# Kernel optimization log

Measured on AMD Instinct MI355X. Metric: run time of the kernel, lower is better.

Reference implementation:

```python
import jax, jax.numpy as jnp
import numpy as np

B, NUM, LQ, LP, H = 8, 4, 128, 512, 512


def setup_inputs() -> dict:
    key = jax.random.key(0)
    k1, k2, k3 = jax.random.split(key, 3)
    return {
        "encode_input1": jax.random.normal(k1, (B, NUM, LQ, H), jnp.float32),
        "encode_input2": jax.random.normal(k2, (B, NUM, LP, H), jnp.float32),
        "input1_mask": jnp.ones((B, NUM, LQ), jnp.int32),
        "input2_mask": jnp.ones((B, NUM, LP), jnp.int32),
        "w": jax.random.normal(k3, (3 * H,), jnp.float32) * (1.0 / np.sqrt(3 * H)),
    }


def reference(encode_input1, encode_input2, input1_mask, input2_mask, w):
    Bb, num_q, Lq, Hh = encode_input1.shape
    _, num_p, Lp, _ = encode_input2.shape
    # num_q == num_p path of the original module
    E_q = encode_input1.reshape(-1, Lq, Hh)            # [BM, Lq, H]
    E_p = encode_input2.reshape(-1, Lp, Hh)            # [BM, Lp, H]
    m_q = input1_mask.reshape(-1, Lq)
    m_p = input2_mask.reshape(-1, Lp)
    # Linear([E_q, E_p, E_q*E_p]) -> scalar decomposes into three terms;
    # avoids materializing the O(Lp*Lq*3H) broadcast-concat tensor.
    w_q, w_p, w_m = w[:Hh], w[Hh:2 * Hh], w[2 * Hh:]
    U = ((E_p @ w_p)[:, :, None]
         + (E_q @ w_q)[:, None, :]
         + jnp.einsum('bph,h,bqh->bpq', E_p, w_m, E_q))   # [BM, Lp, Lq]
    mask = (m_p[:, :, None] * m_q[:, None, :]).astype(bool)
    Um = jnp.where(mask, U, jnp.finfo(U.dtype).min)
    A_p = jnp.where(mask, jax.nn.softmax(Um, axis=2), 0.0)   # row softmax over Lq
    B_p = jnp.where(mask, jax.nn.softmax(Um, axis=1), 0.0)   # col softmax over Lp
    A1 = A_p @ E_q                                   # [BM, Lp, H]
    B1 = jnp.einsum('bpq,bph->bqh', B_p, E_p)        # [BM, Lq, H]
    A2 = A_p @ B1                                    # [BM, Lp, H]
    B2 = jnp.einsum('bpq,bph->bqh', B_p, A1)         # [BM, Lq, H]
    shp_p = (Bb, num_p, Lp, Hh)
    shp_q = (Bb, num_p, Lq, Hh)
    E_p4 = E_p.reshape(shp_p); E_q4 = E_q.reshape(shp_q)
    A1 = A1.reshape(shp_p); A2 = A2.reshape(shp_p)
    B1 = B1.reshape(shp_q); B2 = B2.reshape(shp_q)
    G_q_p = jnp.concatenate([E_p4, A1, A2, E_p4 * A1, E_p4 * A2], axis=-1)
    G_p_q = jnp.concatenate([E_q4, B1, B2, E_q4 * B1, E_q4 * B2], axis=-1)
    G_p_q = G_p_q * input1_mask[..., None].astype(G_p_q.dtype)
    G_q_p = G_q_p * input2_mask[..., None].astype(G_q_p.dtype)
    return (G_p_q, G_q_p)
```

## Files before the change

### kernel.cpp

```cpp
#include <hip/hip_runtime.h>
#include <hip/hip_bf16.h>

#define BBATCH 32
#define LQ 128
#define LP 512
#define HDIM 512
#define GDIM 2560
#define NEG_MAX (-3.402823466e38f)

typedef __attribute__((ext_vector_type(8))) short short8;
typedef __attribute__((ext_vector_type(4))) float f32x4;
typedef __attribute__((ext_vector_type(4))) unsigned short ushort4v;

__device__ inline unsigned short f2bf(float f) {
  union { float f; unsigned int u; } v; v.f = f;
  unsigned int r = v.u + 0x7FFFu + ((v.u >> 16) & 1u);
  return (unsigned short)(r >> 16);
}
__device__ inline float bf2f(unsigned short s) {
  union { unsigned int u; float f; } v; v.u = (unsigned int)s << 16;
  return v.f;
}

__device__ inline void stage128x64(const unsigned short* __restrict__ src, int ld,
                                   int row0, int k0, unsigned short* lds, int t) {
#pragma unroll
  for (int i = 0; i < 4; i++) {
    int o = (t + i * 256) * 16;
    int row = o >> 7, col = (o & 127) >> 1;
    int swz = o ^ ((row & 7) << 4);
    *(short8*)((char*)lds + swz) = *(const short8*)(src + (long)(row0 + row) * ld + k0 + col);
  }
}
__device__ inline void stage64x64_f32(const float* __restrict__ src, int ld,
                                      int row0, int k0, unsigned short* lds, int t) {
#pragma unroll
  for (int i = 0; i < 2; i++) {
    int o = (t + i * 256) * 16;
    int row = o >> 7, col = (o & 127) >> 1;
    int swz = o ^ ((row & 7) << 4);
    const float* p = src + (long)(row0 + row) * ld + k0 + col;
    float4 a = *(const float4*)p;
    float4 b2 = *(const float4*)(p + 4);
    short8 v = {(short)f2bf(a.x), (short)f2bf(a.y), (short)f2bf(a.z), (short)f2bf(a.w),
                (short)f2bf(b2.x), (short)f2bf(b2.y), (short)f2bf(b2.z), (short)f2bf(b2.w)};
    *(short8*)((char*)lds + swz) = v;
  }
}
__device__ inline short8 fragld(const unsigned short* lds, int row, int ks, int fq) {
  return *(const short8*)((const char*)lds + (((row << 7) + ks * 64 + fq * 16) ^ ((row & 7) << 4)));
}

__global__ __launch_bounds__(256) void prep_kernel(
    const float* __restrict__ Ep, const float* __restrict__ Eq,
    const float* __restrict__ w,
    unsigned short* __restrict__ EpT, unsigned short* __restrict__ EqT,
    unsigned short* __restrict__ Eqw,
    float* __restrict__ epv, float* __restrict__ eqv) {
  const int b = blockIdx.y;
  const int bx = blockIdx.x;
  const bool isP = bx < 8;
  const int R = isP ? LP : LQ;
  const int p0 = (isP ? bx : bx - 8) * 64;
  const float* src = isP ? Ep + (long)b * LP * HDIM : Eq + (long)b * LQ * HDIM;
  const float* wb_base = isP ? w + HDIM : w;
  unsigned short* dT = isP ? EpT + (long)b * HDIM * LP : EqT + (long)b * HDIM * LQ;
  unsigned short* dW = isP ? nullptr : Eqw + (long)b * LQ * HDIM;
  float* bias = (isP ? epv + b * LP : eqv + b * LQ) + p0;
  __shared__ float T[64][65];
  const int t = threadIdx.x, c4 = (t & 15) * 4, r = t >> 4;
  float dot[4] = {0.f, 0.f, 0.f, 0.f};
  for (int h0 = 0; h0 < HDIM; h0 += 64) {
    float4 wb = *(const float4*)(wb_base + h0 + c4);
    float4 wm4 = {0, 0, 0, 0};
    if (!isP) wm4 = *(const float4*)(w + 2 * HDIM + h0 + c4);
    __syncthreads();
#pragma unroll
    for (int i = 0; i < 4; i++) {
      int row = r + 16 * i;
      float4 v = *(const float4*)(src + (long)(p0 + row) * HDIM + h0 + c4);
      T[row][c4] = v.x; T[row][c4 + 1] = v.y; T[row][c4 + 2] = v.z; T[row][c4 + 3] = v.w;
      if (!isP) {
        ushort4v ow = {f2bf(v.x * wm4.x), f2bf(v.y * wm4.y), f2bf(v.z * wm4.z), f2bf(v.w * wm4.w)};
        *(ushort4v*)(dW + (long)(p0 + row) * HDIM + h0 + c4) = ow;
      }
      dot[i] += v.x * wb.x + v.y * wb.y + v.z * wb.z + v.w * wb.w;
    }
    __syncthreads();
#pragma unroll
    for (int i = 0; i < 4; i++) {
      int hh = r + 16 * i;
      ushort4v o = {f2bf(T[c4][hh]), f2bf(T[c4 + 1][hh]), f2bf(T[c4 + 2][hh]), f2bf(T[c4 + 3][hh])};
      *(ushort4v*)(dT + (long)(h0 + hh) * R + p0 + c4) = o;
    }
  }
#pragma unroll
  for (int i = 0; i < 4; i++) {
#pragma unroll
    for (int s = 1; s < 16; s <<= 1) dot[i] += __shfl_xor(dot[i], s);
  }
  if ((t & 15) == 0) {
#pragma unroll
    for (int i = 0; i < 4; i++) bias[r + 16 * i] = dot[i];
  }
}

__global__ __launch_bounds__(256) void u_gemm(
    const float* __restrict__ EpF, const unsigned short* __restrict__ Bb,
    const float* __restrict__ epv, const float* __restrict__ eqv,
    const int* __restrict__ maskM, const int* __restrict__ maskN,
    float* __restrict__ UmT, unsigned short* __restrict__ Apb) {
  const int hw = blockIdx.x;
  const int xcd = hw & 7, s_ = hw >> 3;
  const int b = xcd * 4 + (s_ >> 3);
  const int m0 = (s_ & 7) * 64;
  const float* A = EpF + (long)b * LP * HDIM;
  const unsigned short* B = Bb + (long)b * LQ * HDIM;
  __shared__ unsigned short As[4096];
  __shared__ unsigned short Bs[8192];
  __shared__ float smax[2][64], ssum[2][64];
  const int t = threadIdx.x, lane = t & 63, wid = t >> 6;
  const int wm = wid >> 1, wn = wid & 1;
  const int wr = wm * 32, wc = wn * 64;
  const int fr = lane & 15, fq = lane >> 4;
  f32x4 acc[2][4] = {};
  for (int k0 = 0; k0 < HDIM; k0 += 64) {
    stage64x64_f32(A, HDIM, m0, k0, As, t);
    stage128x64(B, HDIM, 0, k0, Bs, t);
    __syncthreads();
#pragma unroll
    for (int ks = 0; ks < 2; ks++) {
      short8 af[2], bfv[4];
#pragma unroll
      for (int i = 0; i < 2; i++) af[i] = fragld(As, wr + i * 16 + fr, ks, fq);
#pragma unroll
      for (int j = 0; j < 4; j++) bfv[j] = fragld(Bs, wc + j * 16 + fr, ks, fq);
#pragma unroll
      for (int i = 0; i < 2; i++)
#pragma unroll
        for (int j = 0; j < 4; j++)
          acc[i][j] = __builtin_amdgcn_mfma_f32_16x16x32_bf16(af[i], bfv[j], acc[i][j], 0, 0, 0);
    }
    __syncthreads();
  }
  const float* ep_b = epv + (long)b * LP;
  const float* eq_b = eqv + (long)b * LQ;
  const int* mM = maskM + (long)b * LP;
  const int* mN = maskN + (long)b * LQ;
  float* UmTB = UmT + (long)b * LQ * LP;
  unsigned short* ApB = Apb + (long)b * LP * LQ;
  float eqc[4]; int mnc[4];
#pragma unroll
  for (int j = 0; j < 4; j++) {
    int col = wc + j * 16 + fr;
    eqc[j] = eq_b[col]; mnc[j] = mN[col];
  }
  float epr[2][4]; int mmr[2][4];
#pragma unroll
  for (int i = 0; i < 2; i++)
#pragma unroll
    for (int r = 0; r < 4; r++) {
      int row = m0 + wr + i * 16 + fq * 4 + r;
      epr[i][r] = ep_b[row]; mmr[i][r] = mM[row];
    }
#pragma unroll
  for (int i = 0; i < 2; i++)
#pragma unroll
    for (int j = 0; j < 4; j++) {
      float4 tv;
#pragma unroll
      for (int r = 0; r < 4; r++) {
        float a = acc[i][j][r];
        bool ok = mmr[i][r] && mnc[j];
        ((float*)&tv)[r] = ok ? a + epr[i][r] : NEG_MAX;
        acc[i][j][r] = ok ? a + eqc[j] : NEG_MAX;
      }
      int col = wc + j * 16 + fr;
      *(float4*)(UmTB + (long)col * LP + m0 + wr + i * 16 + fq * 4) = tv;
    }
  float mx[2][4];
#pragma unroll
  for (int i = 0; i < 2; i++)
#pragma unroll
    for (int r = 0; r < 4; r++) {
      float m = fmaxf(fmaxf(acc[i][0][r], acc[i][1][r]), fmaxf(acc[i][2][r], acc[i][3][r]));
#pragma unroll
      for (int s = 1; s < 16; s <<= 1) m = fmaxf(m, __shfl_xor(m, s));
      mx[i][r] = m;
      if (fr == 0) smax[wn][wr + i * 16 + fq * 4 + r] = m;
    }
  __syncthreads();
#pragma unroll
  for (int i = 0; i < 2; i++)
#pragma unroll
    for (int r = 0; r < 4; r++) {
      int rl = wr + i * 16 + fq * 4 + r;
      mx[i][r] = fmaxf(smax[0][rl], smax[1][rl]);
    }
#pragma unroll
  for (int i = 0; i < 2; i++)
#pragma unroll
    for (int r = 0; r < 4; r++) {
      float s = 0.f;
#pragma unroll
      for (int j = 0; j < 4; j++) {
        float e = __expf(acc[i][j][r] - mx[i][r]);
        acc[i][j][r] = e; s += e;
      }
#pragma unroll
      for (int sh = 1; sh < 16; sh <<= 1) s += __shfl_xor(s, sh);
      if (fr == 0) ssum[wn][wr + i * 16 + fq * 4 + r] = s;
    }
  __syncthreads();
#pragma unroll
  for (int i = 0; i < 2; i++)
#pragma unroll
    for (int r = 0; r < 4; r++) {
      int rl = wr + i * 16 + fq * 4 + r;
      float S = ssum[0][rl] + ssum[1][rl];
      float inv = S > 0.f ? 1.f / S : 0.f;
      int row = m0 + rl;
#pragma unroll
      for (int j = 0; j < 4; j++) {
        int col = wc + j * 16 + fr;
        bool ok = mmr[i][r] && mnc[j];
        ApB[(long)row * LQ + col] = ok ? f2bf(acc[i][j][r] * inv) : 0;
      }
    }
}

__global__ __launch_bounds__(256) void colsoftmaxT_kernel(
    const float* __restrict__ UmT, unsigned short* __restrict__ BpT,
    const int* __restrict__ mp, const int* __restrict__ mq) {
  int wid = blockIdx.x * 4 + (threadIdx.x >> 6);
  int lane = threadIdx.x & 63;
  int b = wid >> 7;
  const float* row = UmT + (long)wid * LP;
  float v[8];
  float m = NEG_MAX;
#pragma unroll
  for (int i = 0; i < 8; i++) { v[i] = row[lane + 64 * i]; m = fmaxf(m, v[i]); }
#pragma unroll
  for (int off = 32; off; off >>= 1) m = fmaxf(m, __shfl_xor(m, off));
  float e[8];
  float s = 0.f;
#pragma unroll
  for (int i = 0; i < 8; i++) { e[i] = __expf(v[i] - m); s += e[i]; }
#pragma unroll
  for (int off = 32; off; off >>= 1) s += __shfl_xor(s, off);
  float inv = s > 0.f ? 1.f / s : 0.f;
  int mqv = mq[wid];
#pragma unroll
  for (int i = 0; i < 8; i++) {
    int p = lane + 64 * i;
    bool ok = mqv && mp[b * LP + p];
    BpT[(long)wid * LP + p] = ok ? f2bf(e[i] * inv) : 0;
  }
}

template <int PHASE>
__global__ __launch_bounds__(256) void gemm_phase(
    const unsigned short* __restrict__ Apb, const unsigned short* __restrict__ BpT,
    const unsigned short* __restrict__ BA, const unsigned short* __restrict__ BB,
    const float* __restrict__ EpF, const float* __restrict__ EqF,
    const int* __restrict__ mp, const int* __restrict__ mq,
    float* __restrict__ out_gqp, float* __restrict__ out_gpq,
    unsigned short* __restrict__ A1T, unsigned short* __restrict__ B1T) {
  const int hw = blockIdx.x;
  const int xcd = hw & 7, s_ = hw >> 3;
  const int b = xcd * 4 + (s_ / 20);
  const int bx = s_ % 20;
  __shared__ __align__(16) char smem[32768];
  unsigned short* As = (unsigned short*)smem;
  unsigned short* Bs = (unsigned short*)(smem + 16384);
  float (*Cs)[132] = (float(*)[132])smem;
  const int t = threadIdx.x, lane = t & 63, wid = t >> 6;
  const int wr = (wid >> 1) * 64, wc = (wid & 1) * 64;
  const int fr = lane & 15, fq = lane >> 4;
  const unsigned short* A; const unsigned short* Bop;
  int K, M, m0, n0;
  float* outBase; const float* Eb; const int* mb;
  unsigned short* Tout;
  if (bx < 4) {
    A = BpT + (long)b * LQ * LP; K = LP; M = LQ; m0 = 0; n0 = bx * 128;
    Bop = BB + (long)b * HDIM * LP;
    outBase = out_gpq + (long)b * LQ * GDIM;
    Eb = EqF + (long)b * LQ * HDIM; mb = mq + (long)b * LQ;
    Tout = (PHASE == 1) ? B1T + (long)b * HDIM * LQ : nullptr;
  } else {
    int idx = bx - 4; m0 = (idx >> 2) * 128; n0 = (idx & 3) * 128;
    A = Apb + (long)b * LP * LQ; K = LQ; M = LP;
    Bop = BA + (long)b * HDIM * LQ;
    outBase = out_gqp + (long)b * LP * GDIM;
    Eb = EpF + (long)b * LP * HDIM; mb = mp + (long)b * LP;
    Tout = (PHASE == 1) ? A1T + (long)b * HDIM * LP : nullptr;
  }
  f32x4 acc[4][4] = {};
  for (int k0 = 0; k0 < K; k0 += 64) {
    stage128x64(A, K, m0, k0, As, t);
    stage128x64(Bop, K, n0, k0, Bs, t);
    __syncthreads();
#pragma unroll
    for (int ks = 0; ks < 2; ks++) {
      short8 af[4], bfv[4];
#pragma unroll
      for (int i = 0; i < 4; i++) {
        af[i] = fragld(As, wr + i * 16 + fr, ks, fq);
        bfv[i] = fragld(Bs, wc + i * 16 + fr, ks, fq);
      }
#pragma unroll
      for (int i = 0; i < 4; i++)
#pragma unroll
        for (int j = 0; j < 4; j++)
          acc[i][j] = __builtin_amdgcn_mfma_f32_16x16x32_bf16(af[i], bfv[j], acc[i][j], 0, 0, 0);
    }
    __syncthreads();
  }
  if (PHASE == 1) {
#pragma unroll
    for (int i = 0; i < 4; i++)
#pragma unroll
      for (int j = 0; j < 4; j++) {
        int col = n0 + wc + j * 16 + fr;
        int row0 = m0 + wr + i * 16 + fq * 4;
        ushort4v o = {f2bf(acc[i][j][0]), f2bf(acc[i][j][1]),
                      f2bf(acc[i][j][2]), f2bf(acc[i][j][3])};
        *(ushort4v*)(Tout + (long)col * M + row0) = o;
      }
  }
  const int band = wid >> 1;
#pragma unroll
  for (int i = 0; i < 4; i++) {
    __syncthreads();
#pragma unroll
    for (int j = 0; j < 4; j++) {
#pragma unroll
      for (int r = 0; r < 4; r++)
        Cs[band * 16 + fq * 4 + r][wc + j * 16 + fr] = acc[i][j][r];
    }
    __syncthreads();
#pragma unroll
    for (int k = 0; k < 4; k++) {
      int slot = t + k * 256;
      int row_l = slot >> 5;
      int c4 = (slot & 31) * 4;
      int bnd = row_l >> 4;
      int r_g = m0 + bnd * 64 + i * 16 + (row_l & 15);
      float mm = (float)mb[r_g];
      f32x4 v = *(f32x4*)&Cs[row_l][c4];
      f32x4 e = *(const f32x4*)(Eb + (long)r_g * HDIM + n0 + c4);
      float* orow = outBase + (long)r_g * GDIM + n0 + c4;
      f32x4 vm = v * mm;
      f32x4 evm = e * vm;
      if (PHASE == 1) {
        __builtin_nontemporal_store(e * mm, (f32x4*)(orow));
        __builtin_nontemporal_store(vm, (f32x4*)(orow + HDIM));
        __builtin_nontemporal_store(evm, (f32x4*)(orow + 3 * HDIM));
      } else {
        __builtin_nontemporal_store(vm, (f32x4*)(orow + 2 * HDIM));
        __builtin_nontemporal_store(evm, (f32x4*)(orow + 4 * HDIM));
      }
    }
  }
}

extern "C" void kernel_launch(void* const* d_in, const int* in_sizes, int n_in,
                              void* d_out, int out_size, void* d_ws, size_t ws_size,
                              hipStream_t stream) {
  const float* Eq = (const float*)d_in[0];
  const float* Ep = (const float*)d_in[1];
  const int* mq = (const int*)d_in[2];
  const int* mp = (const int*)d_in[3];
  const float* w = (const float*)d_in[4];
  float* out = (float*)d_out;
  float* out_gpq = out;
  float* out_gqp = out + (long)BBATCH * LQ * GDIM;

  unsigned short* EpT = (unsigned short*)d_ws;
  unsigned short* EqT = EpT + 32L * 512 * 512;
  unsigned short* Eqw = EqT + 32L * 512 * 128;
  unsigned short* Apb = Eqw + 32L * 128 * 512;
  unsigned short* BpT = Apb + 32L * 512 * 128;
  unsigned short* B1T = BpT + 32L * 128 * 512;
  unsigned short* A1T = B1T + 32L * 512 * 128;
  float* UmT = (float*)(A1T + 32L * 512 * 512);
  float* epb = UmT + 32L * 128 * 512;
  float* eqb2 = epb + 32L * 512;

  prep_kernel<<<dim3(10, BBATCH), 256, 0, stream>>>(
      Ep, Eq, w, EpT, EqT, Eqw, epb, eqb2);

  u_gemm<<<dim3(256), 256, 0, stream>>>(
      Ep, Eqw, epb, eqb2, mp, mq, UmT, Apb);

  colsoftmaxT_kernel<<<BBATCH * LQ / 4, 256, 0, stream>>>(UmT, BpT, mp, mq);

  gemm_phase<1><<<dim3(640), 256, 0, stream>>>(
      Apb, BpT, EqT, EpT, Ep, Eq, mp, mq, out_gqp, out_gpq, A1T, B1T);

  gemm_phase<2><<<dim3(640), 256, 0, stream>>>(
      Apb, BpT, B1T, A1T, Ep, Eq, mp, mq, out_gqp, out_gpq, nullptr, nullptr);
}
```

Before: 107.2 us.

## Reassociate B2 as (Bp^T·Ap)·Eq to drop the A1 intermediate

Computes B2 as (B_p^T A_p) E_q instead of B_p^T (A_p E_q). The small 128x128 product is accumulated alongside B1 in the same K loop, staged in LDS as bf16, and multiplied by Eq^T inside the same block. This removes the A1T bf16 intermediate, which was written and then read back from global memory, and u_gemm now also writes a transposed copy of A_p. The G_p_q blocks now emit all five output slices in one kernel, and A2 moves to a separate smaller kernel. In exchange, the Bp^T·Ap product is recomputed redundantly by each of the four column blocks per batch, those blocks become heavier, which risks load imbalance, and LDS use rises to 64 KB.

```diff
diff --git a/kernel.cpp b/kernel.cpp
--- a/kernel.cpp
+++ b/kernel.cpp
@@ -16,10 +16,6 @@
   union { float f; unsigned int u; } v; v.f = f;
   unsigned int r = v.u + 0x7FFFu + ((v.u >> 16) & 1u);
   return (unsigned short)(r >> 16);
-}
-__device__ inline float bf2f(unsigned short s) {
-  union { unsigned int u; float f; } v; v.u = (unsigned int)s << 16;
-  return v.f;
 }
 
 __device__ inline void stage128x64(const unsigned short* __restrict__ src, int ld,
@@ -109,7 +105,8 @@
     const float* __restrict__ EpF, const unsigned short* __restrict__ Bb,
     const float* __restrict__ epv, const float* __restrict__ eqv,
     const int* __restrict__ maskM, const int* __restrict__ maskN,
-    float* __restrict__ UmT, unsigned short* __restrict__ Apb) {
+    float* __restrict__ UmT, unsigned short* __restrict__ Apb,
+    unsigned short* __restrict__ ApT) {
   const int hw = blockIdx.x;
   const int xcd = hw & 7, s_ = hw >> 3;
   const int b = xcd * 4 + (s_ >> 3);
@@ -149,6 +146,7 @@
   const int* mN = maskN + (long)b * LQ;
   float* UmTB = UmT + (long)b * LQ * LP;
   unsigned short* ApB = Apb + (long)b * LP * LQ;
+  unsigned short* ApTB = ApT + (long)b * LQ * LP;
   float eqc[4]; int mnc[4];
 #pragma unroll
   for (int j = 0; j < 4; j++) {
@@ -215,17 +213,34 @@
 #pragma unroll
   for (int i = 0; i < 2; i++)
 #pragma unroll
-    for (int r = 0; r < 4; r++) {
-      int rl = wr + i * 16 + fq * 4 + r;
+    for (int r0 = 0; r0 < 4; r0++) {
+      int rl = wr + i * 16 + fq * 4 + r0;
       float S = ssum[0][rl] + ssum[1][rl];
       float inv = S > 0.f ? 1.f / S : 0.f;
       int row = m0 + rl;
 #pragma unroll
       for (int j = 0; j < 4; j++) {
         int col = wc + j * 16 + fr;
+        bool ok = mmr[i][r0] && mnc[j];
+        ApB[(long)row * LQ + col] = ok ? f2bf(acc[i][j][r0] * inv) : 0;
+      }
+    }
+#pragma unroll
+  for (int i = 0; i < 2; i++)
+#pragma unroll
+    for (int j = 0; j < 4; j++) {
+      int col = wc + j * 16 + fr;
+      int row0 = m0 + wr + i * 16 + fq * 4;
+      ushort4v o;
+#pragma unroll
+      for (int r = 0; r < 4; r++) {
+        int rl = wr + i * 16 + fq * 4 + r;
+        float S = ssum[0][rl] + ssum[1][rl];
+        float inv = S > 0.f ? 1.f / S : 0.f;
         bool ok = mmr[i][r] && mnc[j];
-        ApB[(long)row * LQ + col] = ok ? f2bf(acc[i][j][r] * inv) : 0;
-      }
+        o[r] = ok ? f2bf(acc[i][j][r] * inv) : 0;
+      }
+      *(ushort4v*)(ApTB + (long)col * LP + row0) = o;
     }
 }
 
@@ -258,18 +273,221 @@
   }
 }
 
-template <int PHASE>
-__global__ __launch_bounds__(256) void gemm_phase(
+__global__ __launch_bounds__(256) void phase_main(
     const unsigned short* __restrict__ Apb, const unsigned short* __restrict__ BpT,
-    const unsigned short* __restrict__ BA, const unsigned short* __restrict__ BB,
+    const unsigned short* __restrict__ ApT, const unsigned short* __restrict__ EqTg,
+    const unsigned short* __restrict__ EqTa, const unsigned short* __restrict__ EpT,
     const float* __restrict__ EpF, const float* __restrict__ EqF,
     const int* __restrict__ mp, const int* __restrict__ mq,
     float* __restrict__ out_gqp, float* __restrict__ out_gpq,
-    unsigned short* __restrict__ A1T, unsigned short* __restrict__ B1T) {
+    unsigned short* __restrict__ B1T) {
   const int hw = blockIdx.x;
   const int xcd = hw & 7, s_ = hw >> 3;
   const int b = xcd * 4 + (s_ / 20);
   const int bx = s_ % 20;
+  __shared__ __align__(16) char smem[65536];
+  unsigned short* As = (unsigned short*)smem;
+  unsigned short* Bs = (unsigned short*)(smem + 16384);
+  unsigned short* Bs2 = (unsigned short*)(smem + 32768);
+  unsigned short* M2l = (unsigned short*)(smem + 49152);
+  float (*Cs)[132] = (float(*)[132])smem;
+  const int t = threadIdx.x, lane = t & 63, wid = t >> 6;
+  const int wr = (wid >> 1) * 64, wc = (wid & 1) * 64;
+  const int fr = lane & 15, fq = lane >> 4;
+
+  if (bx < 4) {
+    const int n0 = bx * 128;
+    const unsigned short* A = BpT + (long)b * LQ * LP;
+    const unsigned short* Bo = EpT + (long)b * HDIM * LP;
+    const unsigned short* Ao = ApT + (long)b * LQ * LP;
+    f32x4 acc1[4][4] = {}, accm[4][4] = {};
+    for (int k0 = 0; k0 < LP; k0 += 64) {
+      stage128x64(A, LP, 0, k0, As, t);
+      stage128x64(Bo, LP, n0, k0, Bs, t);
+      stage128x64(Ao, LP, 0, k0, Bs2, t);
+      __syncthreads();
+#pragma unroll
+      for (int ks = 0; ks < 2; ks++) {
+        short8 af[4], bfv[4], mfv[4];
+#pragma unroll
+        for (int i = 0; i < 4; i++) {
+          af[i] = fragld(As, wr + i * 16 + fr, ks, fq);
+          bfv[i] = fragld(Bs, wc + i * 16 + fr, ks, fq);
+          mfv[i] = fragld(Bs2, wc + i * 16 + fr, ks, fq);
+        }
+#pragma unroll
+        for (int i = 0; i < 4; i++)
+#pragma unroll
+          for (int j = 0; j < 4; j++) {
+            acc1[i][j] = __builtin_amdgcn_mfma_f32_16x16x32_bf16(af[i], bfv[j], acc1[i][j], 0, 0, 0);
+            accm[i][j] = __builtin_amdgcn_mfma_f32_16x16x32_bf16(af[i], mfv[j], accm[i][j], 0, 0, 0);
+          }
+      }
+      __syncthreads();
+    }
+    unsigned short* B1TB = B1T + (long)b * HDIM * LQ;
+#pragma unroll
+    for (int i = 0; i < 4; i++)
+#pragma unroll
+      for (int j = 0; j < 4; j++) {
+        int col = n0 + wc + j * 16 + fr;
+        int row0 = wr + i * 16 + fq * 4;
+        ushort4v o = {f2bf(acc1[i][j][0]), f2bf(acc1[i][j][1]),
+                      f2bf(acc1[i][j][2]), f2bf(acc1[i][j][3])};
+        *(ushort4v*)(B1TB + (long)col * LQ + row0) = o;
+      }
+    const unsigned short* BE = EqTg + (long)b * HDIM * LQ;
+    f32x4 acc2[4][4] = {};
+#pragma unroll
+    for (int ks2 = 0; ks2 < 2; ks2++) {
+      stage128x64(BE, LQ, n0, ks2 * 64, Bs, t);
+      if ((wid & 1) == ks2) {
+#pragma unroll
+        for (int i = 0; i < 4; i++)
+#pragma unroll
+          for (int j = 0; j < 4; j++) {
+            int kk = j * 16 + fr;
+#pragma unroll
+            for (int r = 0; r < 4; r++) {
+              int row = wr + i * 16 + fq * 4 + r;
+              int byte = ((row << 7) + kk * 2) ^ ((row & 7) << 4);
+              *(unsigned short*)((char*)M2l + byte) = f2bf(accm[i][j][r]);
+            }
+          }
+      }
+      __syncthreads();
+#pragma unroll
+      for (int ks = 0; ks < 2; ks++) {
+        short8 af[4], bfv[4];
+#pragma unroll
+        for (int i = 0; i < 4; i++) {
+          af[i] = fragld(M2l, wr + i * 16 + fr, ks, fq);
+          bfv[i] = fragld(Bs, wc + i * 16 + fr, ks, fq);
+        }
+#pragma unroll
+        for (int i = 0; i < 4; i++)
+#pragma unroll
+          for (int j = 0; j < 4; j++)
+            acc2[i][j] = __builtin_amdgcn_mfma_f32_16x16x32_bf16(af[i], bfv[j], acc2[i][j], 0, 0, 0);
+      }
+      __syncthreads();
+    }
+    float* outB = out_gpq + (long)b * LQ * GDIM;
+    const float* Eb = EqF + (long)b * LQ * HDIM;
+    const int* mb = mq + (long)b * LQ;
+    const int band = wid >> 1;
+#pragma unroll
+    for (int i = 0; i < 4; i++) {
+      __syncthreads();
+#pragma unroll
+      for (int j = 0; j < 4; j++)
+#pragma unroll
+        for (int r = 0; r < 4; r++)
+          Cs[band * 16 + fq * 4 + r][wc + j * 16 + fr] = acc1[i][j][r];
+      __syncthreads();
+      f32x4 ev[4]; float mmv[4]; float* orowv[4];
+#pragma unroll
+      for (int k = 0; k < 4; k++) {
+        int slot = t + k * 256;
+        int row_l = slot >> 5;
+        int c4 = (slot & 31) * 4;
+        int bnd = row_l >> 4;
+        int r_g = bnd * 64 + i * 16 + (row_l & 15);
+        mmv[k] = (float)mb[r_g];
+        ev[k] = *(const f32x4*)(Eb + (long)r_g * HDIM + n0 + c4);
+        orowv[k] = outB + (long)r_g * GDIM + n0 + c4;
+        f32x4 v = *(f32x4*)&Cs[row_l][c4];
+        f32x4 vm = v * mmv[k];
+        __builtin_nontemporal_store(ev[k] * mmv[k], (f32x4*)(orowv[k]));
+        __builtin_nontemporal_store(vm, (f32x4*)(orowv[k] + HDIM));
+        __builtin_nontemporal_store(ev[k] * vm, (f32x4*)(orowv[k] + 3 * HDIM));
+      }
+      __syncthreads();
+#pragma unroll
+      for (int j = 0; j < 4; j++)
+#pragma unroll
+        for (int r = 0; r < 4; r++)
+          Cs[band * 16 + fq * 4 + r][wc + j * 16 + fr] = acc2[i][j][r];
+      __syncthreads();
+#pragma unroll
+      for (int k = 0; k < 4; k++) {
+        int slot = t + k * 256;
+        int row_l = slot >> 5;
+        int c4 = (slot & 31) * 4;
+        f32x4 v = *(f32x4*)&Cs[row_l][c4];
+        f32x4 vm = v * mmv[k];
+        __builtin_nontemporal_store(vm, (f32x4*)(orowv[k] + 2 * HDIM));
+        __builtin_nontemporal_store(ev[k] * vm, (f32x4*)(orowv[k] + 4 * HDIM));
+      }
+    }
+  } else {
+    int idx = bx - 4;
+    const int m0 = (idx >> 2) * 128, n0 = (idx & 3) * 128;
+    const unsigned short* A = Apb + (long)b * LP * LQ;
+    const unsigned short* Bo = EqTa + (long)b * HDIM * LQ;
+    f32x4 acc[4][4] = {};
+    for (int k0 = 0; k0 < LQ; k0 += 64) {
+      stage128x64(A, LQ, m0, k0, As, t);
+      stage128x64(Bo, LQ, n0, k0, Bs, t);
+      __syncthreads();
+#pragma unroll
+      for (int ks = 0; ks < 2; ks++) {
+        short8 af[4], bfv[4];
+#pragma unroll
+        for (int i = 0; i < 4; i++) {
+          af[i] = fragld(As, wr + i * 16 + fr, ks, fq);
+          bfv[i] = fragld(Bs, wc + i * 16 + fr, ks, fq);
+        }
+#pragma unroll
+        for (int i = 0; i < 4; i++)
+#pragma unroll
+          for (int j = 0; j < 4; j++)
+            acc[i][j] = __builtin_amdgcn_mfma_f32_16x16x32_bf16(af[i], bfv[j], acc[i][j], 0, 0, 0);
+      }
+      __syncthreads();
+    }
+    float* outB = out_gqp + (long)b * LP * GDIM;
+    const float* Eb = EpF + (long)b * LP * HDIM;
+    const int* mb = mp + (long)b * LP;
+    const int band = wid >> 1;
+#pragma unroll
+    for (int i = 0; i < 4; i++) {
+      __syncthreads();
+#pragma unroll
+      for (int j = 0; j < 4; j++)
+#pragma unroll
+        for (int r = 0; r < 4; r++)
+          Cs[band * 16 + fq * 4 + r][wc + j * 16 + fr] = acc[i][j][r];
+      __syncthreads();
+#pragma unroll
+      for (int k = 0; k < 4; k++) {
+        int slot = t + k * 256;
+        int row_l = slot >> 5;
+        int c4 = (slot & 31) * 4;
+        int bnd = row_l >> 4;
+        int r_g = m0 + bnd * 64 + i * 16 + (row_l & 15);
+        float mm = (float)mb[r_g];
+        f32x4 v = *(f32x4*)&Cs[row_l][c4];
+        f32x4 e = *(const f32x4*)(Eb + (long)r_g * HDIM + n0 + c4);
+        float* orow = outB + (long)r_g * GDIM + n0 + c4;
+        f32x4 vm = v * mm;
+        __builtin_nontemporal_store(e * mm, (f32x4*)(orow));
+        __builtin_nontemporal_store(vm, (f32x4*)(orow + HDIM));
+        __builtin_nontemporal_store(e * vm, (f32x4*)(orow + 3 * HDIM));
+      }
+    }
+  }
+}
+
+__global__ __launch_bounds__(256) void phase_a2(
+    const unsigned short* __restrict__ Apb, const unsigned short* __restrict__ B1T,
+    const float* __restrict__ EpF, const int* __restrict__ mp,
+    float* __restrict__ out_gqp) {
+  const int hw = blockIdx.x;
+  const int xcd = hw & 7, s_ = hw >> 3;
+  const int b = xcd * 4 + (s_ >> 4);
+  const int idx = s_ & 15;
+  const int m0 = (idx >> 2) * 128, n0 = (idx & 3) * 128;
   __shared__ __align__(16) char smem[32768];
   unsigned short* As = (unsigned short*)smem;
   unsigned short* Bs = (unsigned short*)(smem + 16384);
@@ -277,28 +495,12 @@
   const int t = threadIdx.x, lane = t & 63, wid = t >> 6;
   const int wr = (wid >> 1) * 64, wc = (wid & 1) * 64;
   const int fr = lane & 15, fq = lane >> 4;
-  const unsigned short* A; const unsigned short* Bop;
-  int K, M, m0, n0;
-  float* outBase; const float* Eb; const int* mb;
-  unsigned short* Tout;
-  if (bx < 4) {
-    A = BpT + (long)b * LQ * LP; K = LP; M = LQ; m0 = 0; n0 = bx * 128;
-    Bop = BB + (long)b * HDIM * LP;
-    outBase = out_gpq + (long)b * LQ * GDIM;
-    Eb = EqF + (long)b * LQ * HDIM; mb = mq + (long)b * LQ;
-    Tout = (PHASE == 1) ? B1T + (long)b * HDIM * LQ : nullptr;
-  } else {
-    int idx = bx - 4; m0 = (idx >> 2) * 128; n0 = (idx & 3) * 128;
-    A = Apb + (long)b * LP * LQ; K = LQ; M = LP;
-    Bop = BA + (long)b * HDIM * LQ;
-    outBase = out_gqp + (long)b * LP * GDIM;
-    Eb = EpF + (long)b * LP * HDIM; mb = mp + (long)b * LP;
-    Tout = (PHASE == 1) ? A1T + (long)b * HDIM * LP : nullptr;
-  }
+  const unsigned short* A = Apb + (long)b * LP * LQ;
+  const unsigned short* Bo = B1T + (long)b * HDIM * LQ;
   f32x4 acc[4][4] = {};
-  for (int k0 = 0; k0 < K; k0 += 64) {
-    stage128x64(A, K, m0, k0, As, t);
-    stage128x64(Bop, K, n0, k0, Bs, t);
+  for (int k0 = 0; k0 < LQ; k0 += 64) {
+    stage128x64(A, LQ, m0, k0, As, t);
+    stage128x64(Bo, LQ, n0, k0, Bs, t);
     __syncthreads();
 #pragma unroll
     for (int ks = 0; ks < 2; ks++) {
@@ -316,28 +518,18 @@
     }
     __syncthreads();
   }
-  if (PHASE == 1) {
-#pragma unroll
-    for (int i = 0; i < 4; i++)
-#pragma unroll
-      for (int j = 0; j < 4; j++) {
-        int col = n0 + wc + j * 16 + fr;
-        int row0 = m0 + wr + i * 16 + fq * 4;
-        ushort4v o = {f2bf(acc[i][j][0]), f2bf(acc[i][j][1]),
-                      f2bf(acc[i][j][2]), f2bf(acc[i][j][3])};
-        *(ushort4v*)(Tout + (long)col * M + row0) = o;
-      }
-  }
+  float* outB = out_gqp + (long)b * LP * GDIM;
+  const float* Eb = EpF + (long)b * LP * HDIM;
+  const int* mb = mp + (long)b * LP;
   const int band = wid >> 1;
 #pragma unroll
   for (int i = 0; i < 4; i++) {
     __syncthreads();
 #pragma unroll
-    for (int j = 0; j < 4; j++) {
+    for (int j = 0; j < 4; j++)
 #pragma unroll
       for (int r = 0; r < 4; r++)
         Cs[band * 16 + fq * 4 + r][wc + j * 16 + fr] = acc[i][j][r];
-    }
     __syncthreads();
 #pragma unroll
     for (int k = 0; k < 4; k++) {
@@ -349,17 +541,10 @@
       float mm = (float)mb[r_g];
       f32x4 v = *(f32x4*)&Cs[row_l][c4];
       f32x4 e = *(const f32x4*)(Eb + (long)r_g * HDIM + n0 + c4);
-      float* orow = outBase + (long)r_g * GDIM + n0 + c4;
+      float* orow = outB + (long)r_g * GDIM + n0 + c4;
       f32x4 vm = v * mm;
-      f32x4 evm = e * vm;
-      if (PHASE == 1) {
-        __builtin_nontemporal_store(e * mm, (f32x4*)(orow));
-        __builtin_nontemporal_store(vm, (f32x4*)(orow + HDIM));
-        __builtin_nontemporal_store(evm, (f32x4*)(orow + 3 * HDIM));
-      } else {
-        __builtin_nontemporal_store(vm, (f32x4*)(orow + 2 * HDIM));
-        __builtin_nontemporal_store(evm, (f32x4*)(orow + 4 * HDIM));
-      }
+      __builtin_nontemporal_store(vm, (f32x4*)(orow + 2 * HDIM));
+      __builtin_nontemporal_store(e * vm, (f32x4*)(orow + 4 * HDIM));
     }
   }
 }
@@ -380,10 +565,10 @@
   unsigned short* EqT = EpT + 32L * 512 * 512;
   unsigned short* Eqw = EqT + 32L * 512 * 128;
   unsigned short* Apb = Eqw + 32L * 128 * 512;
-  unsigned short* BpT = Apb + 32L * 512 * 128;
+  unsigned short* ApT = Apb + 32L * 512 * 128;
+  unsigned short* BpT = ApT + 32L * 128 * 512;
   unsigned short* B1T = BpT + 32L * 128 * 512;
-  unsigned short* A1T = B1T + 32L * 512 * 128;
-  float* UmT = (float*)(A1T + 32L * 512 * 512);
+  float* UmT = (float*)(B1T + 32L * 512 * 128);
   float* epb = UmT + 32L * 128 * 512;
   float* eqb2 = epb + 32L * 512;
 
@@ -391,13 +576,13 @@
       Ep, Eq, w, EpT, EqT, Eqw, epb, eqb2);
 
   u_gemm<<<dim3(256), 256, 0, stream>>>(
-      Ep, Eqw, epb, eqb2, mp, mq, UmT, Apb);
+      Ep, Eqw, epb, eqb2, mp, mq, UmT, Apb, ApT);
 
   colsoftmaxT_kernel<<<BBATCH * LQ / 4, 256, 0, stream>>>(UmT, BpT, mp, mq);
 
-  gemm_phase<1><<<dim3(640), 256, 0, stream>>>(
-      Apb, BpT, EqT, EpT, Ep, Eq, mp, mq, out_gqp, out_gpq, A1T, B1T);
-
-  gemm_phase<2><<<dim3(640), 256, 0, stream>>>(
-      Apb, BpT, B1T, A1T, Ep, Eq, mp, mq, out_gqp, out_gpq, nullptr, nullptr);
-}
+  phase_main<<<dim3(640), 256, 0, stream>>>(
+      Apb, BpT, ApT, EqT, EqT, EpT, Ep, Eq, mp, mq, out_gqp, out_gpq, B1T);
+
+  phase_a2<<<dim3(512), 256, 0, stream>>>(
+      Apb, B1T, Ep, mp, out_gqp);
+}
```

Result: no change. 108.5 us (+1.2%).
